# Kernel optimization log

Measured on AMD Instinct MI355X. Metric: run time of the kernel, lower is better.

## Reference

```python
import jax, jax.numpy as jnp
import numpy as np

B, T, S, D, VOCAB = 16, 64, 128, 512, 32000


def setup_inputs():
    key = jax.random.key(0)
    ks = jax.random.split(key, 20)
    w = lambda i, shape: jax.random.normal(ks[i], shape, dtype=jnp.float32) * 0.05
    return {
        'words': jax.random.randint(ks[0], (B, T), 0, VOCAB),
        'encoder_output': jax.random.normal(ks[1], (B, S, D), dtype=jnp.float32),
        'pre_h': jax.random.normal(ks[2], (B, D), dtype=jnp.float32),
        'cell': jax.random.normal(ks[3], (B, D), dtype=jnp.float32),
        'emb': w(4, (VOCAB, D)),
        'W_ih': w(5, (4 * D, D)), 'W_hh': w(6, (4 * D, D)),
        'b_ih': w(7, (4 * D,)), 'b_hh': w(8, (4 * D,)),
        'Wh_w': w(9, (D, D)),
        'Ws_w': w(10, (D, D)), 'Ws_b': w(11, (D,)),
        'vt_w': w(12, (D,)),
        'V_w': w(13, (D, 2 * D)), 'V_b': w(14, (D,)),
        'Vp_w': w(15, (VOCAB, D)), 'Vp_b': w(16, (VOCAB,)),
    }


def lstm(xs, h0, c0, W_ih, W_hh, b_ih, b_hh):
    # xs: [T, B, D]; PyTorch LSTM gate order: i, f, g, o
    def step(carry, x_t):
        h, c = carry
        g = x_t @ W_ih.T + b_ih + h @ W_hh.T + b_hh
        i, f, gg, o = jnp.split(g, 4, axis=-1)
        c = jax.nn.sigmoid(f) * c + jax.nn.sigmoid(i) * jnp.tanh(gg)
        h = jax.nn.sigmoid(o) * jnp.tanh(c)
        return (h, c), h
    _, hs = jax.lax.scan(step, (h0, c0), xs)
    return hs


def reference(words, encoder_output, pre_h, cell, emb, W_ih, W_hh, b_ih, b_hh,
              Wh_w, Ws_w, Ws_b, vt_w, V_w, V_b, Vp_w, Vp_b):
    x = emb[words]                                   # [B, T, D]
    hs = lstm(x.transpose(1, 0, 2), pre_h, cell, W_ih, W_hh, b_ih, b_hh)
    out = hs.transpose(1, 0, 2)                      # [B, T, D] decoder states
    wh = encoder_output @ Wh_w.T                     # [B, S, D]
    ws = out @ Ws_w.T + Ws_b                         # [B, T, D]
    # Bahdanau additive attention scores e[b,s,t] = v_t . tanh(wh[b,s] + ws[b,t])
    e = jnp.einsum('bstd,d->bst', jnp.tanh(wh[:, :, None, :] + ws[:, None, :, :]), vt_w)
    a = jax.nn.softmax(e, axis=1)                    # softmax over source positions
    context = jnp.einsum('bst,bsd->btd', a, encoder_output)
    cat = jnp.concatenate([context, out], axis=-1)   # [B, T, 2D]
    return (cat @ V_w.T + V_b) @ Vp_w.T + Vp_b       # [B, T, VOCAB]
```

## Files before the change

kernel.cpp:

```cpp
#include <hip/hip_runtime.h>

#define DEV __device__ __forceinline__

typedef float f32x4 __attribute__((ext_vector_type(4)));
typedef short s16x8 __attribute__((ext_vector_type(8)));
typedef unsigned short u16;
typedef u16 u16x4 __attribute__((ext_vector_type(4)));
typedef u16 u16x8 __attribute__((ext_vector_type(8)));
typedef unsigned int u32x4 __attribute__((ext_vector_type(4)));

constexpr int Bb = 16, Tt = 64, Ss = 128, Dd = 512, Vv = 32000, FD = 2048;

DEV u16 f2bf(float x) {
  unsigned u = __builtin_bit_cast(unsigned, x);
  u = u + 0x7fffu + ((u >> 16) & 1u);
  return (u16)(u >> 16);
}
DEV float bf2f(u16 h) { unsigned u = ((unsigned)h) << 16; return __builtin_bit_cast(float, u); }
DEV float sigm(float x) { return 1.f / (1.f + __expf(-x)); }
DEV float ftanh(float x) {
  x = fminf(15.f, fmaxf(-15.f, x));
  float e = __expf(2.f * x);
  return (e - 1.f) / (e + 1.f);
}

DEV void cvt_plain_one(const float* __restrict__ in, u16* __restrict__ out, int i) {
  float4 v = reinterpret_cast<const float4*>(in)[i];
  u16x4 o;
  o.x = f2bf(v.x); o.y = f2bf(v.y); o.z = f2bf(v.z); o.w = f2bf(v.w);
  reinterpret_cast<u16x4*>(out)[i] = o;
}

DEV void cvt_split_one(const float* __restrict__ in, u16* __restrict__ hi,
                       u16* __restrict__ lo, int i) {
  float4 v = reinterpret_cast<const float4*>(in)[i];
  u16x4 oh, ol;
  float vv[4] = {v.x, v.y, v.z, v.w};
#pragma unroll
  for (int j = 0; j < 4; ++j) {
    u16 h = f2bf(vv[j]);
    oh[j] = h;
    ol[j] = f2bf(vv[j] - bf2f(h));
  }
  reinterpret_cast<u16x4*>(hi)[i] = oh;
  reinterpret_cast<u16x4*>(lo)[i] = ol;
}

__global__ void k_cvt_pre(const float* __restrict__ Wih, u16* __restrict__ Wih_bf, int n0,
                          const float* __restrict__ enc, u16* __restrict__ ench,
                          u16* __restrict__ encl, int n1,
                          const float* __restrict__ Whw, u16* __restrict__ whh,
                          u16* __restrict__ whl, int n2) {
  int total = n0 + n1 + n2;
  int i = blockIdx.x * blockDim.x + threadIdx.x;
  int st = gridDim.x * blockDim.x;
  for (; i < total; i += st) {
    if (i < n0) cvt_plain_one(Wih, Wih_bf, i);
    else if (i < n0 + n1) cvt_split_one(enc, ench, encl, i - n0);
    else cvt_split_one(Whw, whh, whl, i - n0 - n1);
  }
}

__global__ void k_prep(const int* __restrict__ words, const float* __restrict__ emb,
                       u16* __restrict__ xb,
                       const float* __restrict__ pre, unsigned* __restrict__ hp0,
                       const float* __restrict__ bi, const float* __restrict__ bh,
                       float* __restrict__ bsum) {
  int blk = blockIdx.x, tid = threadIdx.x;
  if (blk < Bb * Tt) {
    int row = words[blk];
    int d = tid * 2;
    float2 v = *reinterpret_cast<const float2*>(&emb[(size_t)row * Dd + d]);
    xb[(size_t)blk * Dd + d] = f2bf(v.x);
    xb[(size_t)blk * Dd + d + 1] = f2bf(v.y);
  } else if (blk < Bb * Tt + 32) {
    int i = (blk - Bb * Tt) * 256 + tid;
    float v = pre[i];
    u16 h = f2bf(v);
    u16 l = f2bf(v - bf2f(h));
    hp0[i] = (unsigned)h | ((unsigned)l << 16);
  } else {
    int i = (blk - Bb * Tt - 32) * 256 + tid;
    bsum[i] = bi[i] + bh[i];
  }
}

template <bool BIAS, bool OUTBF, int TERMS>
DEV void gemm_body(u16* ls, int tile, int tid,
                   const u16* __restrict__ A, const u16* __restrict__ Al,
                   const u16* __restrict__ Bm, const u16* __restrict__ Bl,
                   float* __restrict__ Cf, u16* __restrict__ Cb,
                   const float* __restrict__ bias, int M, int N, int K) {
  u16* lsA = ls;
  u16* lsB = ls + 128 * 32;
  u16* lsAl = ls + 2 * 128 * 32;
  u16* lsBl = ls + 3 * 128 * 32;
  const int mt = M >> 7;
  const int tm = (tile % mt) << 7;
  const int tn = (tile / mt) << 7;
  const int wave = tid >> 6, lane = tid & 63;
  const int wr = wave >> 1, wc = wave & 1;
  f32x4 acc[4][4];
#pragma unroll
  for (int i = 0; i < 4; ++i)
#pragma unroll
    for (int j = 0; j < 4; ++j) acc[i][j] = (f32x4){0.f, 0.f, 0.f, 0.f};

  const int lrow = lane >> 2;
  const int lk = (lane & 3) << 3;
  const int fr = lane & 15, fk = (lane >> 4) << 3;

  for (int k0 = 0; k0 < K; k0 += 32) {
#pragma unroll
    for (int r = 0; r < 2; ++r) {
      int rowA = r * 64 + wave * 16;
      size_t goffA = (size_t)(tm + rowA + lrow) * K + k0 + lk;
      size_t goffB = (size_t)(tn + rowA + lrow) * K + k0 + lk;
      __builtin_amdgcn_global_load_lds((const __attribute__((address_space(1))) void*)(A + goffA),
                                       (__attribute__((address_space(3))) void*)&lsA[rowA * 32],
                                       16, 0, 0);
      __builtin_amdgcn_global_load_lds((const __attribute__((address_space(1))) void*)(Bm + goffB),
                                       (__attribute__((address_space(3))) void*)&lsB[rowA * 32],
                                       16, 0, 0);
      if constexpr (TERMS == 3) {
        __builtin_amdgcn_global_load_lds((const __attribute__((address_space(1))) void*)(Al + goffA),
                                         (__attribute__((address_space(3))) void*)&lsAl[rowA * 32],
                                         16, 0, 0);
        __builtin_amdgcn_global_load_lds((const __attribute__((address_space(1))) void*)(Bl + goffB),
                                         (__attribute__((address_space(3))) void*)&lsBl[rowA * 32],
                                         16, 0, 0);
      }
    }
    __syncthreads();
    s16x8 av[4], bv[4];
#pragma unroll
    for (int mi = 0; mi < 4; ++mi)
      av[mi] = *reinterpret_cast<const s16x8*>(&lsA[(wr * 64 + mi * 16 + fr) * 32 + fk]);
#pragma unroll
    for (int ni = 0; ni < 4; ++ni)
      bv[ni] = *reinterpret_cast<const s16x8*>(&lsB[(wc * 64 + ni * 16 + fr) * 32 + fk]);
    if constexpr (TERMS == 3) {
      s16x8 avl[4], bvl[4];
#pragma unroll
      for (int mi = 0; mi < 4; ++mi)
        avl[mi] = *reinterpret_cast<const s16x8*>(&lsAl[(wr * 64 + mi * 16 + fr) * 32 + fk]);
#pragma unroll
      for (int ni = 0; ni < 4; ++ni)
        bvl[ni] = *reinterpret_cast<const s16x8*>(&lsBl[(wc * 64 + ni * 16 + fr) * 32 + fk]);
#pragma unroll
      for (int mi = 0; mi < 4; ++mi)
#pragma unroll
        for (int ni = 0; ni < 4; ++ni) {
          acc[mi][ni] = __builtin_amdgcn_mfma_f32_16x16x32_bf16(av[mi], bv[ni], acc[mi][ni], 0, 0, 0);
          acc[mi][ni] = __builtin_amdgcn_mfma_f32_16x16x32_bf16(av[mi], bvl[ni], acc[mi][ni], 0, 0, 0);
          acc[mi][ni] = __builtin_amdgcn_mfma_f32_16x16x32_bf16(avl[mi], bv[ni], acc[mi][ni], 0, 0, 0);
        }
    } else {
#pragma unroll
      for (int mi = 0; mi < 4; ++mi)
#pragma unroll
        for (int ni = 0; ni < 4; ++ni)
          acc[mi][ni] = __builtin_amdgcn_mfma_f32_16x16x32_bf16(av[mi], bv[ni], acc[mi][ni], 0, 0, 0);
    }
    __syncthreads();
  }

  const int fm = (lane >> 4) << 2;
#pragma unroll
  for (int ni = 0; ni < 4; ++ni) {
    int col = tn + wc * 64 + ni * 16 + fr;
    float badd = 0.f;
    if constexpr (BIAS) badd = bias[col];
#pragma unroll
    for (int mi = 0; mi < 4; ++mi) {
#pragma unroll
      for (int r = 0; r < 4; ++r) {
        int row = tm + wr * 64 + mi * 16 + fm + r;
        size_t idx = (size_t)row * N + col;
        float v = acc[mi][ni][r] + badd;
        if constexpr (OUTBF) Cb[idx] = f2bf(v);
        else Cf[idx] = v;
      }
    }
  }
}

template <bool BIAS, bool OUTBF, int TERMS>
__global__ __launch_bounds__(256) void k_gemm(const u16* __restrict__ A,
                                              const u16* __restrict__ Al,
                                              const u16* __restrict__ Bm,
                                              const u16* __restrict__ Bl,
                                              float* __restrict__ Cf, u16* __restrict__ Cb,
                                              const float* __restrict__ bias,
                                              int M, int N, int K) {
  __shared__ u16 ls[4 * 128 * 32];
  gemm_body<BIAS, OUTBF, TERMS>(ls, blockIdx.x, threadIdx.x, A, Al, Bm, Bl, Cf, Cb, bias, M, N, K);
}

DEV void lstm_body(int w, int tid, float* gls,
                   const float* __restrict__ xg, const float* __restrict__ Whh,
                   const float* __restrict__ cell, unsigned* __restrict__ hpack,
                   u16* __restrict__ out_hi, u16* __restrict__ out_lo,
                   int* __restrict__ flags) {
  const int gi = tid >> 6, lane = tid & 63;
  const int ds0 = w << 4;
  float (*g_lds)[16][16] = (float(*)[16][16])gls;

  const int fr = lane & 15;
  const int fkb = (lane >> 4) << 3;

  s16x8 whi[16], wlo[16];
  {
    const float* wrow = Whh + (size_t)(gi * Dd + ds0 + fr) * Dd;
#pragma unroll
    for (int kc = 0; kc < 16; ++kc) {
      int k = kc * 32 + fkb;
      float4 a = *reinterpret_cast<const float4*>(&wrow[k]);
      float4 b = *reinterpret_cast<const float4*>(&wrow[k + 4]);
      float vv[8] = {a.x, a.y, a.z, a.w, b.x, b.y, b.z, b.w};
#pragma unroll
      for (int j = 0; j < 8; ++j) {
        u16 h = f2bf(vv[j]);
        whi[kc][j] = (short)h;
        wlo[kc][j] = (short)f2bf(vv[j] - bf2f(h));
      }
    }
  }

  const int ub = tid >> 4, ud = tid & 15;
  float c = cell[(size_t)ub * Dd + ds0 + ud];

  for (int t = 0; t < Tt; ++t) {
    float xgv[4];
#pragma unroll
    for (int r = 0; r < 4; ++r) {
      int bb = ((lane >> 4) << 2) + r;
      xgv[r] = xg[(size_t)(bb * Tt + t) * FD + gi * Dd + ds0 + fr];
    }
#pragma unroll
    for (int r = 0; r < 4; ++r) asm volatile("" ::"v"(xgv[r]));

    if (t > 0) {
      if (gi == 0) {
        if (lane < 32 && lane != w) {
          while (__hip_atomic_load(&flags[lane * 32], __ATOMIC_RELAXED,
                                   __HIP_MEMORY_SCOPE_AGENT) < t) {}
          while (__hip_atomic_load(&flags[lane * 32], __ATOMIC_ACQUIRE,
                                   __HIP_MEMORY_SCOPE_AGENT) < t) {}
        }
        __builtin_amdgcn_sched_barrier(0);
      }
      __syncthreads();
    }

    const unsigned* hp = hpack + (size_t)t * (Bb * Dd) + (size_t)fr * Dd;
    f32x4 a0 = (f32x4){0.f, 0.f, 0.f, 0.f};
    f32x4 a1 = a0, a2 = a0;
#pragma unroll
    for (int kc = 0; kc < 16; ++kc) {
      int k = kc * 32 + fkb;
      u32x4 u0 = *reinterpret_cast<const u32x4*>(&hp[k]);
      u32x4 u1 = *reinterpret_cast<const u32x4*>(&hp[k + 4]);
      s16x8 ahi, alo;
#pragma unroll
      for (int j = 0; j < 4; ++j) {
        ahi[j] = (short)(u0[j] & 0xffffu); alo[j] = (short)(u0[j] >> 16);
        ahi[4 + j] = (short)(u1[j] & 0xffffu); alo[4 + j] = (short)(u1[j] >> 16);
      }
      a0 = __builtin_amdgcn_mfma_f32_16x16x32_bf16(ahi, whi[kc], a0, 0, 0, 0);
      a1 = __builtin_amdgcn_mfma_f32_16x16x32_bf16(ahi, wlo[kc], a1, 0, 0, 0);
      a2 = __builtin_amdgcn_mfma_f32_16x16x32_bf16(alo, whi[kc], a2, 0, 0, 0);
    }
#pragma unroll
    for (int r = 0; r < 4; ++r) {
      int bb = ((lane >> 4) << 2) + r;
      g_lds[gi][bb][fr] = a0[r] + a1[r] + a2[r] + xgv[r];
    }
    __syncthreads();
    float iv = g_lds[0][ub][ud], fv = g_lds[1][ub][ud];
    float gv = g_lds[2][ub][ud], ov = g_lds[3][ub][ud];
    c = sigm(fv) * c + sigm(iv) * ftanh(gv);
    float h = sigm(ov) * ftanh(c);
    u16 hh = f2bf(h);
    u16 hl = f2bf(h - bf2f(hh));
    unsigned pk = (unsigned)hh | ((unsigned)hl << 16);
    __hip_atomic_store(&hpack[(size_t)(t + 1) * (Bb * Dd) + ub * Dd + ds0 + ud], pk,
                       __ATOMIC_RELAXED, __HIP_MEMORY_SCOPE_AGENT);
    size_t oidx = (size_t)(ub * Tt + t) * Dd + ds0 + ud;
    out_hi[oidx] = hh;
    out_lo[oidx] = hl;
    __syncthreads();
    if (tid == 0)
      __hip_atomic_store(&flags[w * 32], t + 1, __ATOMIC_RELAXED, __HIP_MEMORY_SCOPE_AGENT);
  }
}

__global__ __launch_bounds__(256) void k_lstm_fused(
    const float* __restrict__ xg, const float* __restrict__ Whh,
    const float* __restrict__ cell, unsigned* __restrict__ hpack,
    u16* __restrict__ out_hi, u16* __restrict__ out_lo, int* __restrict__ flags,
    const u16* __restrict__ enc_hi, const u16* __restrict__ enc_lo,
    const u16* __restrict__ Whw_hi, const u16* __restrict__ Whw_lo,
    float* __restrict__ wh,
    const float* __restrict__ Vp_w, u16* __restrict__ Vp_bf,
    const float* __restrict__ V_w, u16* __restrict__ Vw_bf,
    const float* __restrict__ Ws_w, u16* __restrict__ Wsw_hi, u16* __restrict__ Wsw_lo) {
  __shared__ u16 ls[4 * 128 * 32];
  const int blk = blockIdx.x, tid = threadIdx.x;
  if (blk < 32) {
    lstm_body(blk, tid, (float*)ls, xg, Whh, cell, hpack, out_hi, out_lo, flags);
  } else if (blk < 96) {
    gemm_body<false, false, 3>(ls, blk - 32, tid, enc_hi, enc_lo, Whw_hi, Whw_lo,
                               wh, nullptr, nullptr, 2048, 512, 512);
  } else {
    const int nVp = Vv * Dd / 4, nV = Dd * 2 * Dd / 4, nWs = Dd * Dd / 4;
    int total = nVp + nV + nWs;
    int i = (blk - 96) * 256 + tid;
    int st = 160 * 256;
    for (; i < total; i += st) {
      if (i < nVp) cvt_plain_one(Vp_w, Vp_bf, i);
      else if (i < nVp + nV) cvt_plain_one(V_w, Vw_bf, i - nVp);
      else cvt_split_one(Ws_w, Wsw_hi, Wsw_lo, i - nVp - nV);
    }
  }
}

__global__ __launch_bounds__(256) void k_attn(const float* __restrict__ wh,
                                              const float* __restrict__ wst,
                                              const float* __restrict__ vt,
                                              const float* __restrict__ enc,
                                              const u16* __restrict__ out_hi,
                                              u16* __restrict__ cat) {
  const int tid = threadIdx.x;
  const int wave = tid >> 6, lane = tid & 63;
  const int wid = blockIdx.x * 4 + wave;
  const int b = wid >> 6, t = wid & 63;
  const int d0 = lane << 3;

  float wsv[8], vtv[8];
  {
    const float4* p = reinterpret_cast<const float4*>(&wst[(size_t)(b * Tt + t) * Dd + d0]);
    float4 x = p[0], y = p[1];
    wsv[0] = x.x; wsv[1] = x.y; wsv[2] = x.z; wsv[3] = x.w;
    wsv[4] = y.x; wsv[5] = y.y; wsv[6] = y.z; wsv[7] = y.w;
    const float4* q = reinterpret_cast<const float4*>(&vt[d0]);
    float4 u = q[0], v = q[1];
    vtv[0] = u.x; vtv[1] = u.y; vtv[2] = u.z; vtv[3] = u.w;
    vtv[4] = v.x; vtv[5] = v.y; vtv[6] = v.z; vtv[7] = v.w;
  }
  float e0 = 0.f, e1 = 0.f;
  for (int s = 0; s < Ss; ++s) {
    const float4* p = reinterpret_cast<const float4*>(&wh[(size_t)(b * Ss + s) * Dd + d0]);
    float4 x = p[0], y = p[1];
    float whv[8] = {x.x, x.y, x.z, x.w, y.x, y.y, y.z, y.w};
    float a = 0.f;
#pragma unroll
    for (int j = 0; j < 8; ++j) a += ftanh(whv[j] + wsv[j]) * vtv[j];
#pragma unroll
    for (int off = 32; off; off >>= 1) a += __shfl_xor(a, off);
    if (lane == (s & 63)) { if (s < 64) e0 = a; else e1 = a; }
  }
  float m = fmaxf(e0, e1);
#pragma unroll
  for (int off = 32; off; off >>= 1) m = fmaxf(m, __shfl_xor(m, off));
  float p0 = __expf(e0 - m), p1 = __expf(e1 - m);
  float sum = p0 + p1;
#pragma unroll
  for (int off = 32; off; off >>= 1) sum += __shfl_xor(sum, off);
  float inv = 1.f / sum;
  float a0 = p0 * inv, a1 = p1 * inv;

  float ctx[8] = {0.f, 0.f, 0.f, 0.f, 0.f, 0.f, 0.f, 0.f};
  for (int s = 0; s < Ss; ++s) {
    float as = __shfl(s < 64 ? a0 : a1, s & 63);
    const float4* p = reinterpret_cast<const float4*>(&enc[(size_t)(b * Ss + s) * Dd + d0]);
    float4 x = p[0], y = p[1];
    ctx[0] += as * x.x; ctx[1] += as * x.y; ctx[2] += as * x.z; ctx[3] += as * x.w;
    ctx[4] += as * y.x; ctx[5] += as * y.y; ctx[6] += as * y.z; ctx[7] += as * y.w;
  }
  u16x8 co;
#pragma unroll
  for (int j = 0; j < 8; ++j) co[j] = f2bf(ctx[j]);
  size_t cbase = (size_t)(b * Tt + t) * (2 * Dd);
  *reinterpret_cast<u16x8*>(&cat[cbase + d0]) = co;
  u16x8 ov = *reinterpret_cast<const u16x8*>(&out_hi[(size_t)(b * Tt + t) * Dd + d0]);
  *reinterpret_cast<u16x8*>(&cat[cbase + Dd + d0]) = ov;
}

extern "C" void kernel_launch(void* const* d_in, const int* in_sizes, int n_in,
                              void* d_out, int out_size, void* d_ws, size_t ws_size,
                              hipStream_t stream) {
  const int* words = (const int*)d_in[0];
  const float* enc = (const float*)d_in[1];
  const float* pre_h = (const float*)d_in[2];
  const float* cell = (const float*)d_in[3];
  const float* emb = (const float*)d_in[4];
  const float* W_ih = (const float*)d_in[5];
  const float* W_hh = (const float*)d_in[6];
  const float* b_ih = (const float*)d_in[7];
  const float* b_hh = (const float*)d_in[8];
  const float* Wh_w = (const float*)d_in[9];
  const float* Ws_w = (const float*)d_in[10];
  const float* Ws_b = (const float*)d_in[11];
  const float* vt_w = (const float*)d_in[12];
  const float* V_w = (const float*)d_in[13];
  const float* V_b = (const float*)d_in[14];
  const float* Vp_w = (const float*)d_in[15];
  const float* Vp_b = (const float*)d_in[16];
  float* outp = (float*)d_out;

  char* ws = (char*)d_ws;
  size_t off = 0;
  auto alloc = [&](size_t bytes) {
    char* p = ws + off;
    off = (off + bytes + 255) & ~(size_t)255;
    return p;
  };
  int* flags = (int*)alloc(4096);
  float* xg = (float*)alloc((size_t)Bb * Tt * FD * 4);
  float* wh = (float*)alloc((size_t)Bb * Ss * Dd * 4);
  float* wst = (float*)alloc((size_t)Bb * Tt * Dd * 4);
  unsigned* hpack = (unsigned*)alloc((size_t)(Tt + 1) * Bb * Dd * 4);
  u16* out_hi = (u16*)alloc((size_t)Bb * Tt * Dd * 2);
  u16* out_lo = (u16*)alloc((size_t)Bb * Tt * Dd * 2);
  u16* x_bf = (u16*)alloc((size_t)Bb * Tt * Dd * 2);
  u16* enc_hi = (u16*)alloc((size_t)Bb * Ss * Dd * 2);
  u16* enc_lo = (u16*)alloc((size_t)Bb * Ss * Dd * 2);
  u16* Wih_bf = (u16*)alloc((size_t)FD * Dd * 2);
  u16* Whw_hi = (u16*)alloc((size_t)Dd * Dd * 2);
  u16* Whw_lo = (u16*)alloc((size_t)Dd * Dd * 2);
  u16* Wsw_hi = (u16*)alloc((size_t)Dd * Dd * 2);
  u16* Wsw_lo = (u16*)alloc((size_t)Dd * Dd * 2);
  u16* Vw_bf = (u16*)alloc((size_t)Dd * 2 * Dd * 2);
  u16* Vp_bf = (u16*)alloc((size_t)Vv * Dd * 2);
  u16* cat = (u16*)alloc((size_t)Bb * Tt * 2 * Dd * 2);
  u16* hmid = (u16*)alloc((size_t)Bb * Tt * Dd * 2);
  float* bsum = (float*)alloc((size_t)FD * 4);
  if (off > ws_size) return;

  hipMemsetAsync(flags, 0, 4096, stream);

  k_cvt_pre<<<256, 256, 0, stream>>>(W_ih, Wih_bf, FD * Dd / 4,
                                     enc, enc_hi, enc_lo, Bb * Ss * Dd / 4,
                                     Wh_w, Whw_hi, Whw_lo, Dd * Dd / 4);
  k_prep<<<Bb * Tt + 32 + 8, 256, 0, stream>>>(words, emb, x_bf, pre_h, (unsigned*)hpack,
                                               b_ih, b_hh, bsum);
  k_gemm<true, false, 1><<<8 * 16, 256, 0, stream>>>(x_bf, nullptr, Wih_bf, nullptr,
                                                     xg, nullptr, bsum, 1024, 2048, 512);
  k_lstm_fused<<<256, 256, 0, stream>>>(xg, W_hh, cell, (unsigned*)hpack, out_hi, out_lo,
                                        flags, enc_hi, enc_lo, Whw_hi, Whw_lo, wh,
                                        Vp_w, Vp_bf, V_w, Vw_bf, Ws_w, Wsw_hi, Wsw_lo);
  k_gemm<true, false, 3><<<8 * 4, 256, 0, stream>>>(out_hi, out_lo, Wsw_hi, Wsw_lo,
                                                    wst, nullptr, Ws_b, 1024, 512, 512);
  k_attn<<<256, 256, 0, stream>>>(wh, wst, vt_w, enc, out_hi, cat);
  k_gemm<true, true, 1><<<8 * 4, 256, 0, stream>>>(cat, nullptr, Vw_bf, nullptr,
                                                   nullptr, hmid, V_b, 1024, 512, 1024);
  k_gemm<true, false, 1><<<8 * 250, 256, 0, stream>>>(hmid, nullptr, Vp_bf, nullptr,
                                                      outp, nullptr, Vp_b, 1024, 32000, 512);
}
```

Measured before the change: 592.0 us.

## Merge prep kernels, relax LSTM sync, add LDS-resident logits GEMM

Merges the conversion and prep kernels into a single launch. In the LSTM recurrence it drops the acquire spin, reads h through relaxed 64-bit atomic loads, and publishes the step flag before writing outputs to shorten the critical path. It also replaces the final vocabulary GEMM with a kernel that keeps a 128-column slice of Vp in LDS and streams all 1024 rows past it. Dropping the acquire ordering may rely on hardware coherence behaviour that is not guaranteed, and the new logits kernel uses only 250 blocks with large LDS.

```diff
diff --git a/kernel.cpp b/kernel.cpp
--- a/kernel.cpp
+++ b/kernel.cpp
@@ -5,9 +5,9 @@
 typedef float f32x4 __attribute__((ext_vector_type(4)));
 typedef short s16x8 __attribute__((ext_vector_type(8)));
 typedef unsigned short u16;
+typedef unsigned long long u64;
 typedef u16 u16x4 __attribute__((ext_vector_type(4)));
 typedef u16 u16x8 __attribute__((ext_vector_type(8)));
-typedef unsigned int u32x4 __attribute__((ext_vector_type(4)));
 
 constexpr int Bb = 16, Tt = 64, Ss = 128, Dd = 512, Vv = 32000, FD = 2048;
 
@@ -46,26 +46,16 @@
   reinterpret_cast<u16x4*>(lo)[i] = ol;
 }
 
-__global__ void k_cvt_pre(const float* __restrict__ Wih, u16* __restrict__ Wih_bf, int n0,
-                          const float* __restrict__ enc, u16* __restrict__ ench,
-                          u16* __restrict__ encl, int n1,
-                          const float* __restrict__ Whw, u16* __restrict__ whh,
-                          u16* __restrict__ whl, int n2) {
-  int total = n0 + n1 + n2;
-  int i = blockIdx.x * blockDim.x + threadIdx.x;
-  int st = gridDim.x * blockDim.x;
-  for (; i < total; i += st) {
-    if (i < n0) cvt_plain_one(Wih, Wih_bf, i);
-    else if (i < n0 + n1) cvt_split_one(enc, ench, encl, i - n0);
-    else cvt_split_one(Whw, whh, whl, i - n0 - n1);
-  }
-}
-
-__global__ void k_prep(const int* __restrict__ words, const float* __restrict__ emb,
-                       u16* __restrict__ xb,
-                       const float* __restrict__ pre, unsigned* __restrict__ hp0,
-                       const float* __restrict__ bi, const float* __restrict__ bh,
-                       float* __restrict__ bsum) {
+__global__ void k_pre(const int* __restrict__ words, const float* __restrict__ emb,
+                      u16* __restrict__ xb,
+                      const float* __restrict__ pre, unsigned* __restrict__ hp0,
+                      const float* __restrict__ bi, const float* __restrict__ bh,
+                      float* __restrict__ bsum,
+                      const float* __restrict__ Wih, u16* __restrict__ Wih_bf,
+                      const float* __restrict__ enc, u16* __restrict__ ench,
+                      u16* __restrict__ encl,
+                      const float* __restrict__ Whw, u16* __restrict__ whh,
+                      u16* __restrict__ whl) {
   int blk = blockIdx.x, tid = threadIdx.x;
   if (blk < Bb * Tt) {
     int row = words[blk];
@@ -79,9 +69,19 @@
     u16 h = f2bf(v);
     u16 l = f2bf(v - bf2f(h));
     hp0[i] = (unsigned)h | ((unsigned)l << 16);
-  } else {
+  } else if (blk < Bb * Tt + 40) {
     int i = (blk - Bb * Tt - 32) * 256 + tid;
     bsum[i] = bi[i] + bh[i];
+  } else {
+    const int n0 = FD * Dd / 4, n1 = Bb * Ss * Dd / 4, n2 = Dd * Dd / 4;
+    int total = n0 + n1 + n2;
+    int i = (blk - (Bb * Tt + 40)) * 256 + tid;
+    int st = 256 * 256;
+    for (; i < total; i += st) {
+      if (i < n0) cvt_plain_one(Wih, Wih_bf, i);
+      else if (i < n0 + n1) cvt_split_one(enc, ench, encl, i - n0);
+      else cvt_split_one(Whw, whh, whl, i - n0 - n1);
+    }
   }
 }
 
@@ -245,27 +245,29 @@
         if (lane < 32 && lane != w) {
           while (__hip_atomic_load(&flags[lane * 32], __ATOMIC_RELAXED,
                                    __HIP_MEMORY_SCOPE_AGENT) < t) {}
-          while (__hip_atomic_load(&flags[lane * 32], __ATOMIC_ACQUIRE,
-                                   __HIP_MEMORY_SCOPE_AGENT) < t) {}
         }
         __builtin_amdgcn_sched_barrier(0);
       }
       __syncthreads();
     }
 
-    const unsigned* hp = hpack + (size_t)t * (Bb * Dd) + (size_t)fr * Dd;
+    const u64* hp8 = reinterpret_cast<const u64*>(
+        hpack + (size_t)t * (Bb * Dd) + (size_t)fr * Dd + fkb);
     f32x4 a0 = (f32x4){0.f, 0.f, 0.f, 0.f};
     f32x4 a1 = a0, a2 = a0;
 #pragma unroll
     for (int kc = 0; kc < 16; ++kc) {
-      int k = kc * 32 + fkb;
-      u32x4 u0 = *reinterpret_cast<const u32x4*>(&hp[k]);
-      u32x4 u1 = *reinterpret_cast<const u32x4*>(&hp[k + 4]);
+      u64 q[4];
+#pragma unroll
+      for (int j = 0; j < 4; ++j)
+        q[j] = __hip_atomic_load(&hp8[kc * 16 + j], __ATOMIC_RELAXED,
+                                 __HIP_MEMORY_SCOPE_AGENT);
       s16x8 ahi, alo;
 #pragma unroll
       for (int j = 0; j < 4; ++j) {
-        ahi[j] = (short)(u0[j] & 0xffffu); alo[j] = (short)(u0[j] >> 16);
-        ahi[4 + j] = (short)(u1[j] & 0xffffu); alo[4 + j] = (short)(u1[j] >> 16);
+        unsigned lo32 = (unsigned)q[j], hi32 = (unsigned)(q[j] >> 32);
+        ahi[2 * j] = (short)(lo32 & 0xffffu); alo[2 * j] = (short)(lo32 >> 16);
+        ahi[2 * j + 1] = (short)(hi32 & 0xffffu); alo[2 * j + 1] = (short)(hi32 >> 16);
       }
       a0 = __builtin_amdgcn_mfma_f32_16x16x32_bf16(ahi, whi[kc], a0, 0, 0, 0);
       a1 = __builtin_amdgcn_mfma_f32_16x16x32_bf16(ahi, wlo[kc], a1, 0, 0, 0);
@@ -286,12 +288,12 @@
     unsigned pk = (unsigned)hh | ((unsigned)hl << 16);
     __hip_atomic_store(&hpack[(size_t)(t + 1) * (Bb * Dd) + ub * Dd + ds0 + ud], pk,
                        __ATOMIC_RELAXED, __HIP_MEMORY_SCOPE_AGENT);
+    __syncthreads();
+    if (tid == 0)
+      __hip_atomic_store(&flags[w * 32], t + 1, __ATOMIC_RELAXED, __HIP_MEMORY_SCOPE_AGENT);
     size_t oidx = (size_t)(ub * Tt + t) * Dd + ds0 + ud;
     out_hi[oidx] = hh;
     out_lo[oidx] = hl;
-    __syncthreads();
-    if (tid == 0)
-      __hip_atomic_store(&flags[w * 32], t + 1, __ATOMIC_RELAXED, __HIP_MEMORY_SCOPE_AGENT);
   }
 }
 
@@ -385,6 +387,65 @@
   *reinterpret_cast<u16x8*>(&cat[cbase + d0]) = co;
   u16x8 ov = *reinterpret_cast<const u16x8*>(&out_hi[(size_t)(b * Tt + t) * Dd + d0]);
   *reinterpret_cast<u16x8*>(&cat[cbase + Dd + d0]) = ov;
+}
+
+__global__ __launch_bounds__(256) void k_logits(const u16* __restrict__ hmid,
+                                                const u16* __restrict__ Vp_bf,
+                                                const float* __restrict__ Vp_b,
+                                                float* __restrict__ out) {
+  constexpr int RS = 520;
+  __shared__ u16 lsB[128 * RS];
+  const int n = blockIdx.x, tid = threadIdx.x;
+  const int wave = tid >> 6, lane = tid & 63;
+  const int wr = wave >> 1, wc = wave & 1;
+  const int fr = lane & 15, fk = (lane >> 4) << 3;
+  const int fm = (lane >> 4) << 2;
+
+  for (int r = wave * 32; r < wave * 32 + 32; ++r) {
+    const u16* src = Vp_bf + (size_t)(n * 128 + r) * 512 + lane * 8;
+    __builtin_amdgcn_global_load_lds((const __attribute__((address_space(1))) void*)src,
+                                     (__attribute__((address_space(3))) void*)&lsB[r * RS],
+                                     16, 0, 0);
+  }
+  __syncthreads();
+
+  s16x8 bvc[4];
+  for (int c = 0; c < 8; ++c) {
+    f32x4 acc[4][4];
+#pragma unroll
+    for (int i = 0; i < 4; ++i)
+#pragma unroll
+      for (int j = 0; j < 4; ++j) acc[i][j] = (f32x4){0.f, 0.f, 0.f, 0.f};
+    for (int k0 = 0; k0 < 512; k0 += 32) {
+      s16x8 av[4];
+#pragma unroll
+      for (int mi = 0; mi < 4; ++mi) {
+        size_t arow = (size_t)(c * 128 + wr * 64 + mi * 16 + fr) * 512 + k0 + fk;
+        av[mi] = *reinterpret_cast<const s16x8*>(&hmid[arow]);
+      }
+#pragma unroll
+      for (int ni = 0; ni < 4; ++ni)
+        bvc[ni] = *reinterpret_cast<const s16x8*>(&lsB[(wc * 64 + ni * 16 + fr) * RS + k0 + fk]);
+#pragma unroll
+      for (int mi = 0; mi < 4; ++mi)
+#pragma unroll
+        for (int ni = 0; ni < 4; ++ni)
+          acc[mi][ni] = __builtin_amdgcn_mfma_f32_16x16x32_bf16(av[mi], bvc[ni], acc[mi][ni], 0, 0, 0);
+    }
+#pragma unroll
+    for (int ni = 0; ni < 4; ++ni) {
+      int col = n * 128 + wc * 64 + ni * 16 + fr;
+      float badd = Vp_b[col];
+#pragma unroll
+      for (int mi = 0; mi < 4; ++mi) {
+#pragma unroll
+        for (int r = 0; r < 4; ++r) {
+          int row = c * 128 + wr * 64 + mi * 16 + fm + r;
+          out[(size_t)row * Vv + col] = acc[mi][ni][r] + badd;
+        }
+      }
+    }
+  }
 }
 
 extern "C" void kernel_launch(void* const* d_in, const int* in_sizes, int n_in,
@@ -440,11 +501,10 @@
 
   hipMemsetAsync(flags, 0, 4096, stream);
 
-  k_cvt_pre<<<256, 256, 0, stream>>>(W_ih, Wih_bf, FD * Dd / 4,
-                                     enc, enc_hi, enc_lo, Bb * Ss * Dd / 4,
-                                     Wh_w, Whw_hi, Whw_lo, Dd * Dd / 4);
-  k_prep<<<Bb * Tt + 32 + 8, 256, 0, stream>>>(words, emb, x_bf, pre_h, (unsigned*)hpack,
-                                               b_ih, b_hh, bsum);
+  k_pre<<<Bb * Tt + 40 + 256, 256, 0, stream>>>(words, emb, x_bf, pre_h, (unsigned*)hpack,
+                                                b_ih, b_hh, bsum,
+                                                W_ih, Wih_bf, enc, enc_hi, enc_lo,
+                                                Wh_w, Whw_hi, Whw_lo);
   k_gemm<true, false, 1><<<8 * 16, 256, 0, stream>>>(x_bf, nullptr, Wih_bf, nullptr,
                                                      xg, nullptr, bsum, 1024, 2048, 512);
   k_lstm_fused<<<256, 256, 0, stream>>>(xg, W_hh, cell, (unsigned*)hpack, out_hi, out_lo,
@@ -455,6 +515,5 @@
   k_attn<<<256, 256, 0, stream>>>(wh, wst, vt_w, enc, out_hi, cat);
   k_gemm<true, true, 1><<<8 * 4, 256, 0, stream>>>(cat, nullptr, Vw_bf, nullptr,
                                                    nullptr, hmid, V_b, 1024, 512, 1024);
-  k_gemm<true, false, 1><<<8 * 250, 256, 0, stream>>>(hmid, nullptr, Vp_bf, nullptr,
-                                                      outp, nullptr, Vp_b, 1024, 32000, 512);
-}
+  k_logits<<<250, 256, 0, stream>>>(hmid, Vp_bf, Vp_b, outp);
+}
```

Measured after the change: 859.6 us. 1.45x slower.
